# Kernel optimization log

Hardware: AMD Instinct MI355X
Metric: run time of the kernel (lower is better)

Reference implementation:

```python
import jax, jax.numpy as jnp
import numpy as np

B, L, DM, H, DK, DV, DH = 16, 1024, 512, 8, 64, 64, 2048
FACTOR = 5
EPS = 1e-5


def _ln(x, g, b):
    m = x.mean(-1, keepdims=True)
    v = jnp.mean((x - m) ** 2, axis=-1, keepdims=True)
    return g * (x - m) / jnp.sqrt(v + EPS) + b


def setup_inputs() -> dict:
    key = jax.random.key(0)
    ks = jax.random.split(key, 12)
    w = lambda k, s: jax.random.normal(k, s, jnp.float32) * 0.02
    sample_k = min(FACTOR * int(np.ceil(np.log(L))), L)  # 35
    return {
        "x": jax.random.normal(ks[0], (B, L, DM), jnp.float32),
        "Wq": w(ks[1], (DM, H * DK)), "bq": jnp.zeros((H * DK,), jnp.float32),
        "Wk": w(ks[2], (DM, H * DK)), "bk": jnp.zeros((H * DK,), jnp.float32),
        "Wv": w(ks[3], (DM, H * DV)), "bv": jnp.zeros((H * DV,), jnp.float32),
        "Wo": w(ks[4], (H * DV, DM)), "bo": jnp.zeros((DM,), jnp.float32),
        "g1": jnp.ones((DM,), jnp.float32), "beta1": jnp.zeros((DM,), jnp.float32),
        "W1": w(ks[5], (DM, DH)), "bf1": jnp.zeros((DH,), jnp.float32),
        "W2": w(ks[6], (DH, DM)), "bf2": jnp.zeros((DM,), jnp.float32),
        "g2": jnp.ones((DM,), jnp.float32), "beta2": jnp.zeros((DM,), jnp.float32),
        "index_sample": jax.random.randint(ks[7], (L, sample_k), 0, L),
        "stage": 0,  # eval; mask=False so attn_mask is always False
    }


def _prob_attention(Q, K, V, index_sample):
    # Q,K,V: [B,H,L,D] (Informer ProbAttention, mask_flag=False, eval)
    Bq, Hq, Lq, D = Q.shape
    u = index_sample.shape[1]  # u == U_part since L_Q == L_K
    # sparse sampled scores: K gathered per-query -> [B,H,L,sample_k,D]
    K_sample = K[:, :, index_sample, :]
    QK_sample = jnp.einsum("bhld,bhlsd->bhls", Q, K_sample)
    M = QK_sample.max(-1) - QK_sample.mean(-1)            # [B,H,L] sparsity measure
    _, M_top = jax.lax.top_k(M, u)                         # [B,H,u]
    Q_reduce = jnp.take_along_axis(Q, M_top[..., None], axis=2)  # [B,H,u,D]
    scores = jnp.einsum("bhud,bhld->bhul", Q_reduce, K) / jnp.sqrt(jnp.float32(D))
    attn = jax.nn.softmax(scores, axis=-1)                 # [B,H,u,L]
    # initial context = mean of V over keys, broadcast to all queries
    context = jnp.broadcast_to(V.mean(axis=2, keepdims=True), V.shape)
    bi = jnp.arange(Bq)[:, None, None]
    hi = jnp.arange(Hq)[None, :, None]
    context = context.at[bi, hi, M_top].set(jnp.einsum("bhul,bhld->bhud", attn, V))
    # output_attention=True: uniform 1/L everywhere, true attn at selected queries
    attns = jnp.full((Bq, Hq, Lq, Lq), 1.0 / Lq, dtype=attn.dtype)
    attns = attns.at[bi, hi, M_top].set(attn)
    return context, attns


def reference(x, Wq, bq, Wk, bk, Wv, bv, Wo, bo, g1, beta1, W1, bf1, W2, bf2, g2, beta2, index_sample, stage):
    residual = x
    Q = (x @ Wq + bq).reshape(B, L, H, DK).transpose(0, 2, 1, 3)
    K = (x @ Wk + bk).reshape(B, L, H, DK).transpose(0, 2, 1, 3)
    V = (x @ Wv + bv).reshape(B, L, H, DV).transpose(0, 2, 1, 3)
    ctx, score = _prob_attention(Q, K, V, index_sample)
    ctx = ctx.transpose(0, 2, 1, 3).reshape(B, L, H * DV)
    out = ctx @ Wo + bo
    x1 = _ln(out + residual, g1, beta1)          # dropout = identity (eval)
    ffn = jax.nn.relu(x1 @ W1 + bf1) @ W2 + bf2
    x2 = _ln(ffn + x1, g2, beta2)
    return x2, score
```

## Files before the change

kernel.cpp:

```cpp
#include <hip/hip_runtime.h>
#include <cstdint>
#include <cstddef>

#define Bc 16
#define Lc 1024
#define DMc 512
#define Hc 8
#define DHc 2048
#define Uc 35

#define FILL_BLKS 32768
#define PREP_BLKS (8192 + 4 * 256 + 2 * 1024 + 1)

typedef __attribute__((ext_vector_type(8))) short bf16x8;
typedef __attribute__((ext_vector_type(4))) float f32x4;

__device__ __forceinline__ ushort f2bf(float f) {
    union { float f; uint32_t u; } v; v.f = f;
    uint32_t r = v.u + 0x7FFF + ((v.u >> 16) & 1);
    return (ushort)(r >> 16);
}
__device__ __forceinline__ float bf2f(ushort u) {
    union { uint32_t i; float f; } v; v.i = ((uint32_t)u) << 16; return v.f;
}

__device__ __forceinline__ void glds16(const ushort* g, ushort* l) {
    __builtin_amdgcn_global_load_lds(
        (__attribute__((address_space(1))) void*)(void*)const_cast<ushort*>(g),
        (__attribute__((address_space(3))) void*)l, 16, 0, 0);
}

template<int MODE, int FILL>
__global__ __launch_bounds__(256) void gemm_mfma(
    const ushort* __restrict__ A, const ushort* __restrict__ Bt,
    const float* __restrict__ bias, void* __restrict__ out0,
    int M, int N, int K, int nxb, int nblk, float* __restrict__ fillbuf)
{
    const int tid = threadIdx.x;
    if (FILL && (int)blockIdx.x >= nblk) {
        int fb = blockIdx.x - nblk;
        const float iv = 1.0f / (float)Lc;
        float4 v4 = make_float4(iv, iv, iv, iv);
        size_t i = (size_t)fb * 256 + tid;
        const size_t nth = (size_t)FILL_BLKS * 256;
        float4* pp = reinterpret_cast<float4*>(fillbuf);
        #pragma unroll
        for (int c = 0; c < 4; ++c) pp[i + c * nth] = v4;
        return;
    }

    __shared__ ushort As[2][128 * 32];
    __shared__ ushort Bs[2][128 * 32];
    int wg = blockIdx.x;
    wg = (wg & 7) * (nblk >> 3) + (wg >> 3);
    const int n0 = (wg % nxb) * 128;
    const int m0 = (wg / nxb) * 128;

    const int lane = tid & 63;
    const int wave = tid >> 6;
    const int wr = wave >> 1, wc = wave & 1;
    const int lrow = lane & 15;
    const int lk = (lane >> 4) * 8;

    f32x4 zero = {0.f, 0.f, 0.f, 0.f};
    f32x4 acc[4][4];
    #pragma unroll
    for (int m = 0; m < 4; ++m)
        #pragma unroll
        for (int n = 0; n < 4; ++n) acc[m][n] = zero;

    const int srow = tid >> 2;
    const int skc = (tid & 3) * 8;
    const int ldsb = (tid & 192) * 8;

    auto stage = [&](int k0, int bufi) {
        glds16(A  + (size_t)(m0 + srow) * K + k0 + skc,      &As[bufi][ldsb]);
        glds16(A  + (size_t)(m0 + 64 + srow) * K + k0 + skc, &As[bufi][2048 + ldsb]);
        glds16(Bt + (size_t)(n0 + srow) * K + k0 + skc,      &Bs[bufi][ldsb]);
        glds16(Bt + (size_t)(n0 + 64 + srow) * K + k0 + skc, &Bs[bufi][2048 + ldsb]);
    };

    const int nt = K >> 5;
    stage(0, 0);
    __syncthreads();
    int cur = 0;
    for (int t = 0; t < nt; ++t) {
        if (t + 1 < nt) stage((t + 1) << 5, cur ^ 1);
        bf16x8 af[4], bv[4];
        #pragma unroll
        for (int m = 0; m < 4; ++m)
            af[m] = *reinterpret_cast<const bf16x8*>(&As[cur][(wr * 64 + m * 16 + lrow) * 32 + lk]);
        #pragma unroll
        for (int n = 0; n < 4; ++n)
            bv[n] = *reinterpret_cast<const bf16x8*>(&Bs[cur][(wc * 64 + n * 16 + lrow) * 32 + lk]);
        #pragma unroll
        for (int m = 0; m < 4; ++m)
            #pragma unroll
            for (int n = 0; n < 4; ++n)
                acc[m][n] = __builtin_amdgcn_mfma_f32_16x16x32_bf16(af[m], bv[n], acc[m][n], 0, 0, 0);
        __syncthreads();
        cur ^= 1;
    }

    #pragma unroll
    for (int n = 0; n < 4; ++n) {
        int col = n0 + wc * 64 + n * 16 + lrow;
        float bval = bias[col];
        #pragma unroll
        for (int m = 0; m < 4; ++m) {
            #pragma unroll
            for (int j = 0; j < 4; ++j) {
                int row = m0 + wr * 64 + m * 16 + (lane >> 4) * 4 + j;
                float v = acc[m][n][j] + bval;
                if (MODE == 2) v = fmaxf(v, 0.0f);
                if (MODE == 0)
                    ((float*)out0)[(size_t)row * N + col] = v;
                else
                    ((ushort*)out0)[(size_t)row * N + col] = f2bf(v);
            }
        }
    }
}

__device__ __forceinline__ void tr_tile(
    const float* __restrict__ in, ushort* __restrict__ out,
    int K, int N, int bx, int by, float (*t)[33], int tid)
{
    int n0 = bx * 32, k0 = by * 32;
    int tx = tid & 31, ty = tid >> 5;
    #pragma unroll
    for (int dy = 0; dy < 32; dy += 8)
        t[ty + dy][tx] = in[(size_t)(k0 + ty + dy) * N + n0 + tx];
    __syncthreads();
    #pragma unroll
    for (int dy = 0; dy < 32; dy += 8)
        out[(size_t)(n0 + ty + dy) * K + k0 + tx] = f2bf(t[tx][ty + dy]);
}

__global__ __launch_bounds__(256) void prep_kernel(
    const float* __restrict__ x,
    const float* __restrict__ Wq, const float* __restrict__ Wk,
    const float* __restrict__ Wv, const float* __restrict__ Wo,
    const float* __restrict__ W1, const float* __restrict__ W2,
    const float* __restrict__ bq, const float* __restrict__ bk,
    const float* __restrict__ bv,
    ushort* __restrict__ xbf, ushort* __restrict__ Wqkvt,
    ushort* __restrict__ Wot, ushort* __restrict__ W1t,
    ushort* __restrict__ W2t, float* __restrict__ bcat)
{
    __shared__ float t[32][33];
    const int tid = threadIdx.x;
    int bid = blockIdx.x;
    if (bid < 8192) {
        int i = bid * 256 + tid;
        float4 v = reinterpret_cast<const float4*>(x)[i];
        uint32_t lo = (uint32_t)f2bf(v.x) | ((uint32_t)f2bf(v.y) << 16);
        uint32_t hi = (uint32_t)f2bf(v.z) | ((uint32_t)f2bf(v.w) << 16);
        reinterpret_cast<uint2*>(xbf)[i] = make_uint2(lo, hi);
        return;
    }
    bid -= 8192;
    if (bid < 256) { tr_tile(Wq, Wqkvt,              512, 512, bid & 15, bid >> 4, t, tid); return; }
    bid -= 256;
    if (bid < 256) { tr_tile(Wk, Wqkvt + 512 * 512,  512, 512, bid & 15, bid >> 4, t, tid); return; }
    bid -= 256;
    if (bid < 256) { tr_tile(Wv, Wqkvt + 1024 * 512, 512, 512, bid & 15, bid >> 4, t, tid); return; }
    bid -= 256;
    if (bid < 256) { tr_tile(Wo, Wot,                512, 512, bid & 15, bid >> 4, t, tid); return; }
    bid -= 256;
    if (bid < 1024) { tr_tile(W1, W1t,               512, 2048, bid & 63, bid >> 6, t, tid); return; }
    bid -= 1024;
    if (bid < 1024) { tr_tile(W2, W2t,               2048, 512, bid & 15, bid >> 4, t, tid); return; }
    for (int i = tid; i < 1536; i += 256)
        bcat[i] = (i < 512) ? bq[i] : (i < 1024) ? bk[i - 512] : bv[i - 1024];
}

__global__ __launch_bounds__(256) void compute_M_kernel(
    const ushort* __restrict__ QKV, const int* __restrict__ idx,
    float* __restrict__ Mout)
{
    __shared__ float qs[4][64];
    const int tid = threadIdx.x;
    const int wid = tid >> 6;
    const int lane = tid & 63;
    const int task = blockIdx.x * 4 + wid;
    const int l = task & (Lc - 1);
    const int bh = task >> 10;
    const int h = bh & (Hc - 1);
    const int b = bh >> 3;

    qs[wid][lane] = bf2f(QKV[(size_t)(b * Lc + l) * 1536 + h * 64 + lane]);

    const bool act = lane < Uc;
    int kl = act ? idx[l * Uc + lane] : 0;
    const bf16x8* kr = reinterpret_cast<const bf16x8*>(
        QKV + (size_t)(b * Lc + kl) * 1536 + 512 + h * 64);
    float dot = 0.0f;
    if (act) {
        #pragma unroll
        for (int c = 0; c < 8; ++c) {
            bf16x8 kv = kr[c];
            #pragma unroll
            for (int e = 0; e < 8; ++e)
                dot += qs[wid][c * 8 + e] * bf2f((ushort)kv[e]);
        }
    }
    float mx = act ? dot : -INFINITY;
    float sm = act ? dot : 0.0f;
    #pragma unroll
    for (int off = 32; off; off >>= 1) {
        mx = fmaxf(mx, __shfl_xor(mx, off, 64));
        sm += __shfl_xor(sm, off, 64);
    }
    if (lane == 0) Mout[task] = mx - sm * (1.0f / Uc);
}

__global__ __launch_bounds__(256) void topk_kernel(
    const float* __restrict__ Mvals, int* __restrict__ Mtop)
{
    const int bh = blockIdx.x;
    const int t = threadIdx.x;
    const int lane = t & 63, wid = t >> 6;
    float v[4];
    #pragma unroll
    for (int c = 0; c < 4; ++c) v[c] = Mvals[((size_t)bh << 10) + t + 256 * c];

    __shared__ float cv[4];
    __shared__ int   ci[4];
    __shared__ int   wini;

    for (int j = 0; j < Uc; ++j) {
        float bv = v[0]; int bi = t;
        #pragma unroll
        for (int c = 1; c < 4; ++c)
            if (v[c] > bv) { bv = v[c]; bi = t + 256 * c; }
        #pragma unroll
        for (int off = 32; off; off >>= 1) {
            float ov = __shfl_xor(bv, off, 64);
            int   oi = __shfl_xor(bi, off, 64);
            if (ov > bv || (ov == bv && oi < bi)) { bv = ov; bi = oi; }
        }
        if (lane == 0) { cv[wid] = bv; ci[wid] = bi; }
        __syncthreads();
        if (t == 0) {
            float fv = cv[0]; int fi = ci[0];
            #pragma unroll
            for (int w = 1; w < 4; ++w)
                if (cv[w] > fv || (cv[w] == fv && ci[w] < fi)) { fv = cv[w]; fi = ci[w]; }
            Mtop[bh * Uc + j] = fi;
            wini = fi;
        }
        __syncthreads();
        int wi = wini;
        if ((wi & 255) == t) v[wi >> 8] = -INFINITY;
    }
}

__global__ __launch_bounds__(256) void qk_scores_kernel(
    const ushort* __restrict__ QKV, const int* __restrict__ Mtop,
    float* __restrict__ score)
{
    const int bh = blockIdx.x >> 2;
    const int l0 = (blockIdx.x & 3) * 256;
    const int h = bh & (Hc - 1), b = bh >> 3;
    __shared__ int qpos[Uc];
    __shared__ float Qs[Uc][64];
    const int t = threadIdx.x;
    if (t < Uc) qpos[t] = Mtop[bh * Uc + t];
    __syncthreads();
    for (int i = t; i < Uc * 64; i += 256) {
        int j = i >> 6, d = i & 63;
        Qs[j][d] = bf2f(QKV[(size_t)(b * Lc + qpos[j]) * 1536 + h * 64 + d]);
    }
    __syncthreads();

    const int l = l0 + t;
    const bf16x8* kr = reinterpret_cast<const bf16x8*>(
        QKV + (size_t)(b * Lc + l) * 1536 + 512 + h * 64);
    float acc[Uc] = {};
    #pragma unroll
    for (int c = 0; c < 8; ++c) {
        bf16x8 kv = kr[c];
        float kf[8];
        #pragma unroll
        for (int e = 0; e < 8; ++e) kf[e] = bf2f((ushort)kv[e]);
        #pragma unroll
        for (int j = 0; j < Uc; ++j) {
            float s = 0.0f;
            #pragma unroll
            for (int e = 0; e < 8; ++e) s += Qs[j][c * 8 + e] * kf[e];
            acc[j] += s;
        }
    }
    #pragma unroll
    for (int j = 0; j < Uc; ++j)
        score[((size_t)(bh << 10) + qpos[j]) * Lc + l] = acc[j] * 0.125f;
}

__global__ __launch_bounds__(256) void attn_out_kernel(
    float* __restrict__ score, const ushort* __restrict__ QKV,
    const int* __restrict__ Mtop, ushort* __restrict__ ctx)
{
    const int bh = blockIdx.x;
    const int h = bh & (Hc - 1), b = bh >> 3;
    const int t = threadIdx.x;
    const int d = t & 63, part = t >> 6;

    __shared__ int qpos[Uc];
    __shared__ float mz[Uc][2];
    __shared__ float buf[4][Uc][64];
    __shared__ float vmred[4][64];
    __shared__ float vmf[64];

    if (t < Uc) qpos[t] = Mtop[bh * Uc + t];
    __syncthreads();

    for (int j = part; j < Uc; j += 4) {
        const float* row = score + ((size_t)(bh << 10) + qpos[j]) * Lc;
        float v[16];
        float mx = -INFINITY;
        #pragma unroll
        for (int c = 0; c < 16; ++c) { v[c] = row[c * 64 + d]; mx = fmaxf(mx, v[c]); }
        #pragma unroll
        for (int off = 32; off; off >>= 1) mx = fmaxf(mx, __shfl_xor(mx, off, 64));
        float z = 0.0f;
        #pragma unroll
        for (int c = 0; c < 16; ++c) z += expf(v[c] - mx);
        #pragma unroll
        for (int off = 32; off; off >>= 1) z += __shfl_xor(z, off, 64);
        if (d == 0) { mz[j][0] = mx; mz[j][1] = 1.0f / z; }
    }
    __syncthreads();

    float acc[Uc];
    #pragma unroll
    for (int j = 0; j < Uc; ++j) acc[j] = 0.0f;
    float vm = 0.0f;

    for (int c = 0; c < 4; ++c) {
        const int l0 = part * 256 + c * 64;
        #pragma unroll
        for (int j = 0; j < Uc; ++j) {
            size_t off = ((size_t)(bh << 10) + qpos[j]) * Lc + l0 + d;
            float p = expf(score[off] - mz[j][0]) * mz[j][1];
            buf[part][j][d] = p;
            score[off] = p;
        }
        __syncthreads();
        #pragma unroll 4
        for (int li = 0; li < 64; ++li) {
            float v = bf2f(QKV[((size_t)(b << 10) + l0 + li) * 1536 + 1024 + h * 64 + d]);
            vm += v;
            #pragma unroll
            for (int j = 0; j < Uc; ++j) acc[j] += buf[part][j][li] * v;
        }
        __syncthreads();
    }

    #pragma unroll
    for (int j = 0; j < Uc; ++j) buf[part][j][d] = acc[j];
    vmred[part][d] = vm;
    __syncthreads();
    if (t < 64) vmf[t] = (vmred[0][t] + vmred[1][t] + vmred[2][t] + vmred[3][t]) * (1.0f / Lc);
    __syncthreads();

    const int dcol = (t & 15) * 4;
    ushort4 vmu;
    vmu.x = f2bf(vmf[dcol + 0]); vmu.y = f2bf(vmf[dcol + 1]);
    vmu.z = f2bf(vmf[dcol + 2]); vmu.w = f2bf(vmf[dcol + 3]);
    for (int li = 0; li < 64; ++li) {
        int l = (t >> 4) + li * 16;
        *reinterpret_cast<ushort4*>(ctx + ((size_t)(b << 10) + l) * 512 + h * 64 + dcol) = vmu;
    }
    __syncthreads();

    for (int idx = t; idx < Uc * 64; idx += 256) {
        int j = idx >> 6, d2 = idx & 63;
        float s = buf[0][j][d2] + buf[1][j][d2] + buf[2][j][d2] + buf[3][j][d2];
        ctx[((size_t)(b << 10) + qpos[j]) * 512 + h * 64 + d2] = f2bf(s);
    }
}

template<int A_BF, int B_BF, int OUT_BF>
__global__ __launch_bounds__(256) void ln_kernel(
    const void* __restrict__ a, const void* __restrict__ bsrc,
    const float* __restrict__ g, const float* __restrict__ beta,
    void* __restrict__ y)
{
    const int row = blockIdx.x;
    const int t = threadIdx.x;
    float a0, a1, b0, b1;
    if (A_BF) {
        uint32_t u = ((const uint32_t*)a)[(size_t)row * 256 + t];
        a0 = bf2f((ushort)(u & 0xffff)); a1 = bf2f((ushort)(u >> 16));
    } else {
        float2 f = ((const float2*)a)[(size_t)row * 256 + t];
        a0 = f.x; a1 = f.y;
    }
    if (B_BF) {
        uint32_t u = ((const uint32_t*)bsrc)[(size_t)row * 256 + t];
        b0 = bf2f((ushort)(u & 0xffff)); b1 = bf2f((ushort)(u >> 16));
    } else {
        float2 f = ((const float2*)bsrc)[(size_t)row * 256 + t];
        b0 = f.x; b1 = f.y;
    }
    float v0 = a0 + b0, v1 = a1 + b1;
    __shared__ float red[256];
    red[t] = v0 + v1; __syncthreads();
    for (int s = 128; s; s >>= 1) { if (t < s) red[t] += red[t + s]; __syncthreads(); }
    float mean = red[0] * (1.0f / DMc);
    __syncthreads();
    float d0 = v0 - mean, d1 = v1 - mean;
    red[t] = d0 * d0 + d1 * d1; __syncthreads();
    for (int s = 128; s; s >>= 1) { if (t < s) red[t] += red[t + s]; __syncthreads(); }
    float inv = rsqrtf(red[0] * (1.0f / DMc) + 1e-5f);
    float2 gv = ((const float2*)g)[t];
    float2 bt = ((const float2*)beta)[t];
    float o0 = gv.x * d0 * inv + bt.x;
    float o1 = gv.y * d1 * inv + bt.y;
    if (OUT_BF) {
        uint32_t u = (uint32_t)f2bf(o0) | ((uint32_t)f2bf(o1) << 16);
        ((uint32_t*)y)[(size_t)row * 256 + t] = u;
    } else {
        ((float2*)y)[(size_t)row * 256 + t] = make_float2(o0, o1);
    }
}

extern "C" void kernel_launch(void* const* d_in, const int* in_sizes, int n_in,
                              void* d_out, int out_size, void* d_ws, size_t ws_size,
                              hipStream_t stream)
{
    const float* x     = (const float*)d_in[0];
    const float* Wq    = (const float*)d_in[1];
    const float* bq    = (const float*)d_in[2];
    const float* Wk    = (const float*)d_in[3];
    const float* bk    = (const float*)d_in[4];
    const float* Wv    = (const float*)d_in[5];
    const float* bv    = (const float*)d_in[6];
    const float* Wo    = (const float*)d_in[7];
    const float* bo    = (const float*)d_in[8];
    const float* g1    = (const float*)d_in[9];
    const float* beta1 = (const float*)d_in[10];
    const float* W1    = (const float*)d_in[11];
    const float* bf1   = (const float*)d_in[12];
    const float* W2    = (const float*)d_in[13];
    const float* bf2   = (const float*)d_in[14];
    const float* g2    = (const float*)d_in[15];
    const float* beta2 = (const float*)d_in[16];
    const int* index_sample = (const int*)d_in[17];

    const size_t NTOK = (size_t)Bc * Lc;
    const size_t QKV_SZ = NTOK * DMc;
    const size_t HID_SZ = NTOK * DHc;

    char* p = (char*)d_ws;
    auto alloc = [&](size_t bytes) { char* r = p; p += (bytes + 255) & ~(size_t)255; return r; };
    ushort* QKVbf  = (ushort*)alloc(NTOK * 1536 * 2);
    ushort* hidden = (ushort*)alloc(HID_SZ * 2);
    ushort* xbf    = (ushort*)alloc(QKV_SZ * 2);
    ushort* ctxbf  = (ushort*)alloc(QKV_SZ * 2);
    ushort* x1bf   = (ushort*)alloc(QKV_SZ * 2);
    ushort* projbf = (ushort*)alloc(QKV_SZ * 2);
    ushort* ffnbf  = (ushort*)alloc(QKV_SZ * 2);
    ushort* Wqkvt  = (ushort*)alloc((size_t)1536 * 512 * 2);
    ushort* Wot    = (ushort*)alloc((size_t)512 * 512 * 2);
    ushort* W1t    = (ushort*)alloc((size_t)512 * 2048 * 2);
    ushort* W2t    = (ushort*)alloc((size_t)512 * 2048 * 2);
    float*  bcat   = (float*) alloc(1536 * 4);
    float*  Mbuf   = (float*) alloc((size_t)Bc * Hc * Lc * 4);
    int*    Mtop   = (int*)   alloc((size_t)Bc * Hc * 64 * 4);

    float* x2_out    = (float*)d_out;
    float* score_out = x2_out + QKV_SZ;

    dim3 blk(256);

    prep_kernel<<<PREP_BLKS, blk, 0, stream>>>(
        x, Wq, Wk, Wv, Wo, W1, W2, bq, bk, bv,
        xbf, Wqkvt, Wot, W1t, W2t, bcat);

    gemm_mfma<1, 1><<<12 * 128 + FILL_BLKS, blk, 0, stream>>>(
        xbf, Wqkvt, bcat, QKVbf, (int)NTOK, 1536, 512, 12, 12 * 128, score_out);

    compute_M_kernel<<<(Bc * Hc * Lc) / 4, blk, 0, stream>>>(QKVbf, index_sample, Mbuf);
    topk_kernel<<<Bc * Hc, blk, 0, stream>>>(Mbuf, Mtop);

    qk_scores_kernel<<<Bc * Hc * 4, blk, 0, stream>>>(QKVbf, Mtop, score_out);
    attn_out_kernel<<<Bc * Hc, blk, 0, stream>>>(score_out, QKVbf, Mtop, ctxbf);

    gemm_mfma<1, 0><<<4 * 128, blk, 0, stream>>>(
        ctxbf, Wot, bo, projbf, (int)NTOK, 512, 512, 4, 4 * 128, nullptr);
    ln_kernel<1, 1, 1><<<(int)NTOK, blk, 0, stream>>>(projbf, xbf, g1, beta1, x1bf);

    gemm_mfma<2, 0><<<16 * 128, blk, 0, stream>>>(
        x1bf, W1t, bf1, hidden, (int)NTOK, 2048, 512, 16, 16 * 128, nullptr);
    gemm_mfma<1, 0><<<4 * 128, blk, 0, stream>>>(
        hidden, W2t, bf2, ffnbf, (int)NTOK, 512, 2048, 4, 4 * 128, nullptr);
    ln_kernel<1, 1, 0><<<(int)NTOK, blk, 0, stream>>>(ffnbf, x1bf, g2, beta2, x2_out);
}
```

Measured before the change: 685.9 us.

## Skip uniform fill on selected rows and move fill into FFN GEMMs

Before, the 1/L fill of the full attention-score tensor ran alongside the QKV GEMM and wrote every row, including the rows that qk_scores later overwrites. Now a row-selection mask is zeroed in prep, set by topk, and the fill is split across the two FFN GEMM launches. It skips the selected rows and uses nontemporal stores. This removes the redundant writes and lets the large store stream overlap with the FFN GEMMs instead of the QKV GEMM. The cost is an extra 512KB mask buffer plus its zeroing and reads, and a heavier FFN GEMM launch.

```diff
diff --git a/kernel.cpp b/kernel.cpp
--- a/kernel.cpp
+++ b/kernel.cpp
@@ -9,8 +9,8 @@
 #define DHc 2048
 #define Uc 35
 
-#define FILL_BLKS 32768
-#define PREP_BLKS (8192 + 4 * 256 + 2 * 1024 + 1)
+#define FILL_BLKS 16384
+#define PREP_BLKS (8192 + 4 * 256 + 2 * 1024 + 1 + 128)
 
 typedef __attribute__((ext_vector_type(8))) short bf16x8;
 typedef __attribute__((ext_vector_type(4))) float f32x4;
@@ -34,18 +34,21 @@
 __global__ __launch_bounds__(256) void gemm_mfma(
     const ushort* __restrict__ A, const ushort* __restrict__ Bt,
     const float* __restrict__ bias, void* __restrict__ out0,
-    int M, int N, int K, int nxb, int nblk, float* __restrict__ fillbuf)
+    int M, int N, int K, int nxb, int nblk,
+    float* __restrict__ fillbuf, const int* __restrict__ rowsel, int fill_base)
 {
     const int tid = threadIdx.x;
     if (FILL && (int)blockIdx.x >= nblk) {
-        int fb = blockIdx.x - nblk;
+        int fb = (blockIdx.x - nblk) + fill_base;
         const float iv = 1.0f / (float)Lc;
-        float4 v4 = make_float4(iv, iv, iv, iv);
-        size_t i = (size_t)fb * 256 + tid;
-        const size_t nth = (size_t)FILL_BLKS * 256;
-        float4* pp = reinterpret_cast<float4*>(fillbuf);
-        #pragma unroll
-        for (int c = 0; c < 4; ++c) pp[i + c * nth] = v4;
+        f32x4 v4 = {iv, iv, iv, iv};
+        #pragma unroll
+        for (int r = 0; r < 4; ++r) {
+            int row = fb * 4 + r;
+            if (rowsel[row] == 0)
+                __builtin_nontemporal_store(
+                    v4, reinterpret_cast<f32x4*>(fillbuf + (size_t)row * Lc) + tid);
+        }
         return;
     }
 
@@ -146,7 +149,8 @@
     const float* __restrict__ bv,
     ushort* __restrict__ xbf, ushort* __restrict__ Wqkvt,
     ushort* __restrict__ Wot, ushort* __restrict__ W1t,
-    ushort* __restrict__ W2t, float* __restrict__ bcat)
+    ushort* __restrict__ W2t, float* __restrict__ bcat,
+    int* __restrict__ rowsel)
 {
     __shared__ float t[32][33];
     const int tid = threadIdx.x;
@@ -171,8 +175,14 @@
     if (bid < 1024) { tr_tile(W1, W1t,               512, 2048, bid & 63, bid >> 6, t, tid); return; }
     bid -= 1024;
     if (bid < 1024) { tr_tile(W2, W2t,               2048, 512, bid & 15, bid >> 4, t, tid); return; }
-    for (int i = tid; i < 1536; i += 256)
-        bcat[i] = (i < 512) ? bq[i] : (i < 1024) ? bk[i - 512] : bv[i - 1024];
+    bid -= 1024;
+    if (bid < 1) {
+        for (int i = tid; i < 1536; i += 256)
+            bcat[i] = (i < 512) ? bq[i] : (i < 1024) ? bk[i - 512] : bv[i - 1024];
+        return;
+    }
+    bid -= 1;
+    reinterpret_cast<uint4*>(rowsel)[bid * 256 + tid] = make_uint4(0, 0, 0, 0);
 }
 
 __global__ __launch_bounds__(256) void compute_M_kernel(
@@ -216,7 +226,8 @@
 }
 
 __global__ __launch_bounds__(256) void topk_kernel(
-    const float* __restrict__ Mvals, int* __restrict__ Mtop)
+    const float* __restrict__ Mvals, int* __restrict__ Mtop,
+    int* __restrict__ rowsel)
 {
     const int bh = blockIdx.x;
     const int t = threadIdx.x;
@@ -248,6 +259,7 @@
             for (int w = 1; w < 4; ++w)
                 if (cv[w] > fv || (cv[w] == fv && ci[w] < fi)) { fv = cv[w]; fi = ci[w]; }
             Mtop[bh * Uc + j] = fi;
+            rowsel[(bh << 10) + fi] = 1;
             wini = fi;
         }
         __syncthreads();
@@ -469,6 +481,7 @@
     float*  bcat   = (float*) alloc(1536 * 4);
     float*  Mbuf   = (float*) alloc((size_t)Bc * Hc * Lc * 4);
     int*    Mtop   = (int*)   alloc((size_t)Bc * Hc * 64 * 4);
+    int*    rowsel = (int*)   alloc((size_t)Bc * Hc * Lc * 4);
 
     float* x2_out    = (float*)d_out;
     float* score_out = x2_out + QKV_SZ;
@@ -477,24 +490,28 @@
 
     prep_kernel<<<PREP_BLKS, blk, 0, stream>>>(
         x, Wq, Wk, Wv, Wo, W1, W2, bq, bk, bv,
-        xbf, Wqkvt, Wot, W1t, W2t, bcat);
-
-    gemm_mfma<1, 1><<<12 * 128 + FILL_BLKS, blk, 0, stream>>>(
-        xbf, Wqkvt, bcat, QKVbf, (int)NTOK, 1536, 512, 12, 12 * 128, score_out);
+        xbf, Wqkvt, Wot, W1t, W2t, bcat, rowsel);
+
+    gemm_mfma<1, 0><<<12 * 128, blk, 0, stream>>>(
+        xbf, Wqkvt, bcat, QKVbf, (int)NTOK, 1536, 512, 12, 12 * 128,
+        nullptr, nullptr, 0);
 
     compute_M_kernel<<<(Bc * Hc * Lc) / 4, blk, 0, stream>>>(QKVbf, index_sample, Mbuf);
-    topk_kernel<<<Bc * Hc, blk, 0, stream>>>(Mbuf, Mtop);
+    topk_kernel<<<Bc * Hc, blk, 0, stream>>>(Mbuf, Mtop, rowsel);
 
     qk_scores_kernel<<<Bc * Hc * 4, blk, 0, stream>>>(QKVbf, Mtop, score_out);
     attn_out_kernel<<<Bc * Hc, blk, 0, stream>>>(score_out, QKVbf, Mtop, ctxbf);
 
     gemm_mfma<1, 0><<<4 * 128, blk, 0, stream>>>(
-        ctxbf, Wot, bo, projbf, (int)NTOK, 512, 512, 4, 4 * 128, nullptr);
+        ctxbf, Wot, bo, projbf, (int)NTOK, 512, 512, 4, 4 * 128,
+        nullptr, nullptr, 0);
     ln_kernel<1, 1, 1><<<(int)NTOK, blk, 0, stream>>>(projbf, xbf, g1, beta1, x1bf);
 
-    gemm_mfma<2, 0><<<16 * 128, blk, 0, stream>>>(
-        x1bf, W1t, bf1, hidden, (int)NTOK, 2048, 512, 16, 16 * 128, nullptr);
-    gemm_mfma<1, 0><<<4 * 128, blk, 0, stream>>>(
-        hidden, W2t, bf2, ffnbf, (int)NTOK, 512, 2048, 4, 4 * 128, nullptr);
+    gemm_mfma<2, 1><<<16 * 128 + FILL_BLKS, blk, 0, stream>>>(
+        x1bf, W1t, bf1, hidden, (int)NTOK, 2048, 512, 16, 16 * 128,
+        score_out, rowsel, 0);
+    gemm_mfma<1, 1><<<4 * 128 + FILL_BLKS, blk, 0, stream>>>(
+        hidden, W2t, bf2, ffnbf, (int)NTOK, 512, 2048, 4, 4 * 128,
+        score_out, rowsel, FILL_BLKS);
     ln_kernel<1, 1, 0><<<(int)NTOK, blk, 0, stream>>>(ffnbf, x1bf, g2, beta2, x2_out);
 }
```

Result: faster. 577.7 us (-15.8%).
